# Performance work log

Hardware: AMD Instinct MI355X
Metric: run time of the kernel (lower is better)

The kernel has to match this reference:

```python
import jax, jax.numpy as jnp
import numpy as np

TAU = 0.1
MASK_VAL = 1e9


def setup_inputs() -> dict:
    key = jax.random.key(0)
    ka, kb = jax.random.split(key)
    B, D = 4096, 512
    return {
        "view_a": jax.random.normal(ka, (B, D), dtype=jnp.float32),
        "view_b": jax.random.normal(kb, (B, D), dtype=jnp.float32),
    }


def _l2norm(x):
    return x / jnp.maximum(jnp.linalg.norm(x, axis=-1, keepdims=True), 1e-12)


def reference(view_a, view_b):
    a = _l2norm(view_a)
    b = _l2norm(view_b)
    B = a.shape[0]
    labels = jnp.arange(B)  # start_i = 0 (single device)
    mask = jnp.eye(B, dtype=a.dtype) * MASK_VAL

    logits_aa = a @ a.T / TAU - mask
    logits_bb = b @ b.T / TAU - mask
    logits_ab = a @ b.T / TAU
    logits_ba = b @ a.T / TAU

    full_a = jnp.concatenate([logits_ab, logits_aa], axis=1)  # [B, 2B]
    full_b = jnp.concatenate([logits_ba, logits_bb], axis=1)

    def ce(logits):
        logp = jax.nn.log_softmax(logits, axis=-1)
        return -jnp.mean(jnp.take_along_axis(logp, labels[:, None], axis=-1))

    loss = (ce(full_a) + ce(full_b)) / 2

    pred = jnp.argmax(full_a, axis=-1)
    acc = 100.0 * jnp.sum(pred == labels) / B
    return loss, acc
```

## Files before the change

kernel.cpp:

```cpp
#include <hip/hip_runtime.h>
#include <stdint.h>


#define BN 4096
#define DK 512
#define NEG_BIG -1e30f
#define SCL 0.15625f
#define SCL2 0.225396744f
#define C2 14.4269504f
#define TILE_BYTES (64 * DK)
#define NCHUNK 32

typedef __attribute__((ext_vector_type(16))) float floatx16;
typedef __attribute__((ext_vector_type(8))) int intx8;

__global__ void __launch_bounds__(256) prep_kernel(
    const float* __restrict__ A, const float* __restrict__ Bv,
    unsigned char* __restrict__ Gn, float* __restrict__ diag,
    float* __restrict__ out, float* __restrict__ zbase,
    float* __restrict__ mbase) {
  const int gtid = blockIdx.x * 256 + threadIdx.x;
  if (gtid < 2) out[gtid] = 0.0f;
  for (int idx = gtid; idx < (NCHUNK + 64) * 8192; idx += 1024 * 256)
    zbase[idx] = 0.0f;
  for (int idx = gtid; idx < (NCHUNK + 32) * 4096; idx += 1024 * 256)
    mbase[idx] = NEG_BIG;

  const int w = threadIdx.x >> 6, lane = threadIdx.x & 63;
  const int row = blockIdx.x * 4 + w;
  const float4* pa4 = (const float4*)(A + (size_t)row * DK);
  const float4* pb4 = (const float4*)(Bv + (size_t)row * DK);
  float4 a0 = pa4[lane * 2], a1 = pa4[lane * 2 + 1];
  float4 b0 = pb4[lane * 2], b1 = pb4[lane * 2 + 1];
  float ssa = a0.x * a0.x + a0.y * a0.y + a0.z * a0.z + a0.w * a0.w +
              a1.x * a1.x + a1.y * a1.y + a1.z * a1.z + a1.w * a1.w;
  float ssb = b0.x * b0.x + b0.y * b0.y + b0.z * b0.z + b0.w * b0.w +
              b1.x * b1.x + b1.y * b1.y + b1.z * b1.z + b1.w * b1.w;
  float sab = a0.x * b0.x + a0.y * b0.y + a0.z * b0.z + a0.w * b0.w +
              a1.x * b1.x + a1.y * b1.y + a1.z * b1.z + a1.w * b1.w;
#pragma unroll
  for (int off = 32; off > 0; off >>= 1) {
    ssa += __shfl_xor(ssa, off);
    ssb += __shfl_xor(ssb, off);
    sab += __shfl_xor(sab, off);
  }
  float na = fmaxf(sqrtf(ssa), 1e-12f);
  float nb = fmaxf(sqrtf(ssb), 1e-12f);
  const float s = 8.0f;
  float sa = s / na, sb = s / nb;
  const int doff = (lane >> 2) * 32 + (lane & 1) * 16 + ((lane >> 1) & 1) * 8;
  {
    int v0 = __builtin_amdgcn_cvt_pk_fp8_f32(a0.x * sa, a0.y * sa, 0, false);
    v0 = __builtin_amdgcn_cvt_pk_fp8_f32(a0.z * sa, a0.w * sa, v0, true);
    int v1 = __builtin_amdgcn_cvt_pk_fp8_f32(a1.x * sa, a1.y * sa, 0, false);
    v1 = __builtin_amdgcn_cvt_pk_fp8_f32(a1.z * sa, a1.w * sa, v1, true);
    int2 pv; pv.x = v0; pv.y = v1;
    *(int2*)(Gn + (size_t)row * DK + doff) = pv;
  }
  {
    int v0 = __builtin_amdgcn_cvt_pk_fp8_f32(b0.x * sb, b0.y * sb, 0, false);
    v0 = __builtin_amdgcn_cvt_pk_fp8_f32(b0.z * sb, b0.w * sb, v0, true);
    int v1 = __builtin_amdgcn_cvt_pk_fp8_f32(b1.x * sb, b1.y * sb, 0, false);
    v1 = __builtin_amdgcn_cvt_pk_fp8_f32(b1.z * sb, b1.w * sb, v1, true);
    int2 pv; pv.x = v0; pv.y = v1;
    *(int2*)(Gn + (size_t)(BN + row) * DK + doff) = pv;
  }
  if (lane == 0) diag[row] = (sab / (na * nb)) * 10.0f;
}

__global__ void __launch_bounds__(256, 2) tiles_kernel(
    const unsigned char* __restrict__ Gn,
    float* __restrict__ pRS, float* __restrict__ pCS,
    float* __restrict__ pRM, float* __restrict__ pCM) {
  __shared__ __align__(16) unsigned char smem[TILE_BYTES + 4096];

  int bid = blockIdx.x, I = 0;
  for (;;) {
    const int nc = (131 - 2 * I) >> 2;
    if (bid < nc) break;
    bid -= nc; ++I;
  }
  const int chunk = bid;
  const int j0 = 2 * I + chunk * 4;
  const int ntiles = min(4, 128 - 2 * I - chunk * 4);

  const int tid = threadIdx.x;
  const int lane = tid & 63, w = tid >> 6;
  const int n5 = lane & 31, h = lane >> 5;
  const int rbase = I * 128 + w * 32;

  intx8 aw[8];
  {
    const unsigned char* p = Gn + (size_t)(rbase + n5) * DK + h * 16;
#pragma unroll
    for (int i = 0; i < 8; ++i) {
      int4 c0 = *(const int4*)(p + i * 64);
      int4 c1 = *(const int4*)(p + i * 64 + 32);
      intx8 v = {c0.x, c0.y, c0.z, c0.w, c1.x, c1.y, c1.z, c1.w};
      aw[i] = v;
    }
  }

  auto stage = [&](int j) {
    const int cb = j * 64;
#pragma unroll
    for (int ii = 0; ii < 8; ++ii) {
      const int cp = w * 8 + ii;
      const int cl = cp * 2 + h;
      const unsigned char* src =
          Gn + (size_t)(cb + cl) * DK + ((n5 ^ (cl & 31)) * 16);
      __builtin_amdgcn_global_load_lds(
          (const __attribute__((address_space(1))) void*)src,
          (__attribute__((address_space(3))) void*)(smem + cp * 1024),
          16, 0, 0);
    }
  };

  float l[16], mxr[16];
#pragma unroll
  for (int r = 0; r < 16; ++r) { l[r] = 0.f; mxr[r] = NEG_BIG; }

  float* T = (float*)(smem + TILE_BYTES);

#pragma unroll 1
  for (int t = 0; t < ntiles; ++t) {
    const int j = j0 + t;
    stage(j);
    __syncthreads();

    floatx16 acc[2];
#pragma unroll
    for (int cs = 0; cs < 2; ++cs)
#pragma unroll
      for (int r = 0; r < 16; ++r) acc[cs][r] = 0.f;

    const unsigned char* bbase = smem + (size_t)n5 * DK;
#pragma unroll
    for (int i = 0; i < 8; ++i) {
      const int p1 = ((4 * i + h) ^ n5) * 16;
      const int p2 = ((4 * i + 2 + h) ^ n5) * 16;
#pragma unroll
      for (int cs = 0; cs < 2; ++cs) {
        int4 b0 = *(const int4*)(bbase + cs * 32 * DK + p1);
        int4 b1 = *(const int4*)(bbase + cs * 32 * DK + p2);
        intx8 bw = {b0.x, b0.y, b0.z, b0.w, b1.x, b1.y, b1.z, b1.w};
        acc[cs] = __builtin_amdgcn_mfma_scale_f32_32x32x64_f8f6f4(
            aw[i], bw, acc[cs], 0, 0, 0, 0x7F7F7F7F, 0, 0x7F7F7F7F);
      }
    }

    const int cbase = j * 64;
    const bool diagp = ((j >> 1) == I);
    const bool lblp = (I < 32) && (j >= 64);
    const int colg0 = cbase + n5, colg1 = cbase + 32 + n5;
    float csum0 = 0.f, csum1 = 0.f, cmax0 = NEG_BIG, cmax1 = NEG_BIG;

#define EPI_BODY(EXCL0_EXPR, EXCL1_EXPR)                                    \
  _Pragma("unroll")                                                         \
  for (int r = 0; r < 16; ++r) {                                            \
    const int rowg = rbase + (r & 3) + 8 * (r >> 2) + 4 * h;                \
    (void)rowg;                                                             \
    {                                                                       \
      const float v = acc[0][r];                                            \
      const bool excl = (EXCL0_EXPR);                                       \
      const float e = excl ? 0.f : exp2f(fmaf(v, SCL2, -C2));               \
      const float vm = excl ? NEG_BIG : v;                                  \
      l[r] += e; mxr[r] = fmaxf(mxr[r], vm);                                \
      csum0 += e; cmax0 = fmaxf(cmax0, vm);                                 \
    }                                                                       \
    {                                                                       \
      const float v = acc[1][r];                                            \
      const bool excl = (EXCL1_EXPR);                                       \
      const float e = excl ? 0.f : exp2f(fmaf(v, SCL2, -C2));               \
      const float vm = excl ? NEG_BIG : v;                                  \
      l[r] += e; mxr[r] = fmaxf(mxr[r], vm);                                \
      csum1 += e; cmax1 = fmaxf(cmax1, vm);                                 \
    }                                                                       \
  }

    if (diagp) {
      EPI_BODY(colg0 <= rowg, colg1 <= rowg)
    } else if (lblp) {
      EPI_BODY(colg0 == rowg + BN, colg1 == rowg + BN)
    } else {
      EPI_BODY(false, false)
    }
#undef EPI_BODY

    csum0 += __shfl_xor(csum0, 32);
    csum1 += __shfl_xor(csum1, 32);
    cmax0 = fmaxf(cmax0, __shfl_xor(cmax0, 32));
    cmax1 = fmaxf(cmax1, __shfl_xor(cmax1, 32));
    float* cps = T;
    float* cpm = T + 256;
    if (h == 0) {
      cps[w * 64 + n5] = csum0; cps[w * 64 + 32 + n5] = csum1;
      cpm[w * 64 + n5] = cmax0; cpm[w * 64 + 32 + n5] = cmax1;
    }
    __syncthreads();
    if (tid < 64) {
      const float s =
          cps[tid] + cps[64 + tid] + cps[128 + tid] + cps[192 + tid];
      pCS[(size_t)I * 8192 + cbase + tid] = s;
      if (j < 64) {
        const float m = fmaxf(fmaxf(cpm[tid], cpm[64 + tid]),
                              fmaxf(cpm[128 + tid], cpm[192 + tid]));
        pCM[(size_t)I * 4096 + cbase + tid] = m;
      }
    }
  }

#pragma unroll
  for (int off = 1; off < 32; off <<= 1)
#pragma unroll
    for (int r = 0; r < 16; ++r) l[r] += __shfl_xor(l[r], off);
  if (I < 32) {
#pragma unroll
    for (int off = 1; off < 32; off <<= 1)
#pragma unroll
      for (int r = 0; r < 16; ++r)
        mxr[r] = fmaxf(mxr[r], __shfl_xor(mxr[r], off));
  }
  if (n5 == 0) {
#pragma unroll
    for (int r = 0; r < 16; ++r) {
      const int rowg = rbase + (r & 3) + 8 * (r >> 2) + 4 * h;
      pRS[(size_t)chunk * 8192 + rowg] = l[r];
      if (I < 32) pRM[(size_t)chunk * 4096 + rowg] = mxr[r];
    }
  }
}

__global__ void __launch_bounds__(256) finalize_kernel(
    const float* __restrict__ pRS, const float* __restrict__ pCS,
    const float* __restrict__ pRM, const float* __restrict__ pCM,
    const float* __restrict__ diag, float* __restrict__ out) {
  const int i = blockIdx.x * 256 + threadIdx.x;
  float SA = 0.f, SB = 0.f, MA = NEG_BIG;
  for (int s = 0; s < NCHUNK; ++s) {
    SA += pRS[(size_t)s * 8192 + i];
    SB += pRS[(size_t)s * 8192 + BN + i];
  }
  for (int s = 0; s < 64; ++s) {
    SA += pCS[(size_t)s * 8192 + i];
    SB += pCS[(size_t)s * 8192 + BN + i];
  }
  for (int s = 0; s < NCHUNK; ++s) MA = fmaxf(MA, pRM[(size_t)s * 4096 + i]);
  for (int s = 0; s < 32; ++s)     MA = fmaxf(MA, pCM[(size_t)s * 4096 + i]);
  MA *= SCL;

  const float d = diag[i];
  const float eL = exp2f(fmaf(d, 1.44269504f, -C2));
  float lseA = 10.0f + logf(SA + eL);
  float lseB = 10.0f + logf(SB + eL);
  float lossi = (lseA - d) + (lseB - d);
  float corr = (d >= MA) ? 1.f : 0.f;
#pragma unroll
  for (int off = 32; off > 0; off >>= 1) {
    lossi += __shfl_xor(lossi, off);
    corr += __shfl_xor(corr, off);
  }
  __shared__ float sred[2][4];
  if ((threadIdx.x & 63) == 0) {
    int w = threadIdx.x >> 6;
    sred[0][w] = lossi; sred[1][w] = corr;
  }
  __syncthreads();
  if (threadIdx.x == 0) {
    float ls = sred[0][0] + sred[0][1] + sred[0][2] + sred[0][3];
    float cs = sred[1][0] + sred[1][1] + sred[1][2] + sred[1][3];
    atomicAdd(&out[0], ls * (1.0f / 8192.0f));
    atomicAdd(&out[1], cs * (100.0f / 4096.0f));
  }
}

extern "C" void kernel_launch(void* const* d_in, const int* in_sizes, int n_in,
                              void* d_out, int out_size, void* d_ws, size_t ws_size,
                              hipStream_t stream) {
  const float* A = (const float*)d_in[0];
  const float* Bv = (const float*)d_in[1];
  unsigned char* Gn = (unsigned char*)d_ws;
  float* diag = (float*)(Gn + (size_t)8192 * DK);
  float* pRS = diag + BN;
  float* pCS = pRS + NCHUNK * 8192;
  float* pRM = pCS + 64 * 8192;
  float* pCM = pRM + NCHUNK * 4096;
  float* out = (float*)d_out;

  prep_kernel<<<BN / 4, 256, 0, stream>>>(A, Bv, Gn, diag, out, pRS, pRM);
  tiles_kernel<<<1056, 256, 0, stream>>>(Gn, pRS, pCS, pRM, pCM);
  finalize_kernel<<<BN / 256, 256, 0, stream>>>(pRS, pCS, pRM, pCM, diag, out);
}
```

Baseline: 118.4 us.

## Replace per-chunk partial buffers with global atomic row sums and maxima

The partial row/column sum and max buffers are replaced by single global arrays updated with atomicAdd and an order-preserving encoded atomicMax. This removes the large zero/fill initialisation in prep and the multi-pass reduction in finalize. Work per block drops from four tiles to two, which roughly doubles the grid to 2080 blocks for better load balance. In exchange it adds atomic contention and a nondeterministic summation order.

```diff
diff --git a/kernel.cpp b/kernel.cpp
--- a/kernel.cpp
+++ b/kernel.cpp
@@ -9,22 +9,29 @@
 #define SCL2 0.225396744f
 #define C2 14.4269504f
 #define TILE_BYTES (64 * DK)
-#define NCHUNK 32
+#define NBLK2 2080
 
 typedef __attribute__((ext_vector_type(16))) float floatx16;
 typedef __attribute__((ext_vector_type(8))) int intx8;
+
+__device__ __forceinline__ unsigned encf(float f) {
+  unsigned u = __float_as_uint(f);
+  return ((int)u < 0) ? ~u : (u | 0x80000000u);
+}
+__device__ __forceinline__ float decf(unsigned u) {
+  return (u & 0x80000000u) ? __uint_as_float(u & 0x7FFFFFFFu)
+                           : __uint_as_float(~u);
+}
 
 __global__ void __launch_bounds__(256) prep_kernel(
     const float* __restrict__ A, const float* __restrict__ Bv,
     unsigned char* __restrict__ Gn, float* __restrict__ diag,
-    float* __restrict__ out, float* __restrict__ zbase,
-    float* __restrict__ mbase) {
+    float* __restrict__ out, float* __restrict__ SAB,
+    unsigned* __restrict__ MaxEnc) {
   const int gtid = blockIdx.x * 256 + threadIdx.x;
   if (gtid < 2) out[gtid] = 0.0f;
-  for (int idx = gtid; idx < (NCHUNK + 64) * 8192; idx += 1024 * 256)
-    zbase[idx] = 0.0f;
-  for (int idx = gtid; idx < (NCHUNK + 32) * 4096; idx += 1024 * 256)
-    mbase[idx] = NEG_BIG;
+  if (gtid < 2 * BN) SAB[gtid] = 0.0f;
+  if (gtid < BN) MaxEnc[gtid] = encf(NEG_BIG);
 
   const int w = threadIdx.x >> 6, lane = threadIdx.x & 63;
   const int row = blockIdx.x * 4 + w;
@@ -70,19 +77,17 @@
 
 __global__ void __launch_bounds__(256, 2) tiles_kernel(
     const unsigned char* __restrict__ Gn,
-    float* __restrict__ pRS, float* __restrict__ pCS,
-    float* __restrict__ pRM, float* __restrict__ pCM) {
-  __shared__ __align__(16) unsigned char smem[TILE_BYTES + 4096];
+    float* __restrict__ SAB, unsigned* __restrict__ MaxEnc) {
+  __shared__ __align__(16) unsigned char smem[TILE_BYTES + 2048];
 
   int bid = blockIdx.x, I = 0;
   for (;;) {
-    const int nc = (131 - 2 * I) >> 2;
+    const int nc = 64 - I;
     if (bid < nc) break;
     bid -= nc; ++I;
   }
   const int chunk = bid;
-  const int j0 = 2 * I + chunk * 4;
-  const int ntiles = min(4, 128 - 2 * I - chunk * 4);
+  const int j0 = 2 * I + chunk * 2;
 
   const int tid = threadIdx.x;
   const int lane = tid & 63, w = tid >> 6;
@@ -123,7 +128,7 @@
   float* T = (float*)(smem + TILE_BYTES);
 
 #pragma unroll 1
-  for (int t = 0; t < ntiles; ++t) {
+  for (int t = 0; t < 2; ++t) {
     const int j = j0 + t;
     stage(j);
     __syncthreads();
@@ -201,11 +206,11 @@
     if (tid < 64) {
       const float s =
           cps[tid] + cps[64 + tid] + cps[128 + tid] + cps[192 + tid];
-      pCS[(size_t)I * 8192 + cbase + tid] = s;
+      atomicAdd(&SAB[cbase + tid], s);
       if (j < 64) {
         const float m = fmaxf(fmaxf(cpm[tid], cpm[64 + tid]),
                               fmaxf(cpm[128 + tid], cpm[192 + tid]));
-        pCM[(size_t)I * 4096 + cbase + tid] = m;
+        atomicMax(&MaxEnc[cbase + tid], encf(m));
       }
     }
   }
@@ -225,29 +230,19 @@
 #pragma unroll
     for (int r = 0; r < 16; ++r) {
       const int rowg = rbase + (r & 3) + 8 * (r >> 2) + 4 * h;
-      pRS[(size_t)chunk * 8192 + rowg] = l[r];
-      if (I < 32) pRM[(size_t)chunk * 4096 + rowg] = mxr[r];
+      atomicAdd(&SAB[rowg], l[r]);
+      if (I < 32) atomicMax(&MaxEnc[rowg], encf(mxr[r]));
     }
   }
 }
 
 __global__ void __launch_bounds__(256) finalize_kernel(
-    const float* __restrict__ pRS, const float* __restrict__ pCS,
-    const float* __restrict__ pRM, const float* __restrict__ pCM,
+    const float* __restrict__ SAB, const unsigned* __restrict__ MaxEnc,
     const float* __restrict__ diag, float* __restrict__ out) {
   const int i = blockIdx.x * 256 + threadIdx.x;
-  float SA = 0.f, SB = 0.f, MA = NEG_BIG;
-  for (int s = 0; s < NCHUNK; ++s) {
-    SA += pRS[(size_t)s * 8192 + i];
-    SB += pRS[(size_t)s * 8192 + BN + i];
-  }
-  for (int s = 0; s < 64; ++s) {
-    SA += pCS[(size_t)s * 8192 + i];
-    SB += pCS[(size_t)s * 8192 + BN + i];
-  }
-  for (int s = 0; s < NCHUNK; ++s) MA = fmaxf(MA, pRM[(size_t)s * 4096 + i]);
-  for (int s = 0; s < 32; ++s)     MA = fmaxf(MA, pCM[(size_t)s * 4096 + i]);
-  MA *= SCL;
+  const float SA = SAB[i];
+  const float SB = SAB[BN + i];
+  const float MA = decf(MaxEnc[i]) * SCL;
 
   const float d = diag[i];
   const float eL = exp2f(fmaf(d, 1.44269504f, -C2));
@@ -281,13 +276,11 @@
   const float* Bv = (const float*)d_in[1];
   unsigned char* Gn = (unsigned char*)d_ws;
   float* diag = (float*)(Gn + (size_t)8192 * DK);
-  float* pRS = diag + BN;
-  float* pCS = pRS + NCHUNK * 8192;
-  float* pRM = pCS + 64 * 8192;
-  float* pCM = pRM + NCHUNK * 4096;
+  float* SAB = diag + BN;
+  unsigned* MaxEnc = (unsigned*)(SAB + 2 * BN);
   float* out = (float*)d_out;
 
-  prep_kernel<<<BN / 4, 256, 0, stream>>>(A, Bv, Gn, diag, out, pRS, pRM);
-  tiles_kernel<<<1056, 256, 0, stream>>>(Gn, pRS, pCS, pRM, pCM);
-  finalize_kernel<<<BN / 256, 256, 0, stream>>>(pRS, pCS, pRM, pCM, diag, out);
-}
+  prep_kernel<<<BN / 4, 256, 0, stream>>>(A, Bv, Gn, diag, out, SAB, MaxEnc);
+  tiles_kernel<<<NBLK2, 256, 0, stream>>>(Gn, SAB, MaxEnc);
+  finalize_kernel<<<BN / 256, 256, 0, stream>>>(SAB, MaxEnc, diag, out);
+}
```

After: 152.5 us. 28.8% more time.

## Widen tile chunks to eight per block and parallelize finalize reduction

Applied to the files above, without the earlier changes.

Each tiles block now processes up to eight column tiles instead of four, halving the block count and the number of row partial-sum slices. The row-stat smem scratch shrinks accordingly. The finalize kernel splits each row's partial reduction across eight lanes with shuffle combining and launches more blocks, so the serial per-thread loop over partial slices is shorter. Fewer, longer tile blocks may reduce load balance across CUs and lengthen the tail.

```diff
diff --git a/kernel.cpp b/kernel.cpp
--- a/kernel.cpp
+++ b/kernel.cpp
@@ -9,7 +9,8 @@
 #define SCL2 0.225396744f
 #define C2 14.4269504f
 #define TILE_BYTES (64 * DK)
-#define NCHUNK 32
+#define NRS 16
+#define NBLK 544
 
 typedef __attribute__((ext_vector_type(16))) float floatx16;
 typedef __attribute__((ext_vector_type(8))) int intx8;
@@ -21,9 +22,9 @@
     float* __restrict__ mbase) {
   const int gtid = blockIdx.x * 256 + threadIdx.x;
   if (gtid < 2) out[gtid] = 0.0f;
-  for (int idx = gtid; idx < (NCHUNK + 64) * 8192; idx += 1024 * 256)
+  for (int idx = gtid; idx < (NRS + 64) * 8192; idx += 1024 * 256)
     zbase[idx] = 0.0f;
-  for (int idx = gtid; idx < (NCHUNK + 32) * 4096; idx += 1024 * 256)
+  for (int idx = gtid; idx < (NRS + 32) * 4096; idx += 1024 * 256)
     mbase[idx] = NEG_BIG;
 
   const int w = threadIdx.x >> 6, lane = threadIdx.x & 63;
@@ -72,17 +73,17 @@
     const unsigned char* __restrict__ Gn,
     float* __restrict__ pRS, float* __restrict__ pCS,
     float* __restrict__ pRM, float* __restrict__ pCM) {
-  __shared__ __align__(16) unsigned char smem[TILE_BYTES + 4096];
+  __shared__ __align__(16) unsigned char smem[TILE_BYTES + 2048];
 
   int bid = blockIdx.x, I = 0;
   for (;;) {
-    const int nc = (131 - 2 * I) >> 2;
+    const int nc = (135 - 2 * I) >> 3;
     if (bid < nc) break;
     bid -= nc; ++I;
   }
   const int chunk = bid;
-  const int j0 = 2 * I + chunk * 4;
-  const int ntiles = min(4, 128 - 2 * I - chunk * 4);
+  const int j0 = 2 * I + chunk * 8;
+  const int ntiles = min(8, 128 - 2 * I - chunk * 8);
 
   const int tid = threadIdx.x;
   const int lane = tid & 63, w = tid >> 6;
@@ -235,26 +236,43 @@
     const float* __restrict__ pRS, const float* __restrict__ pCS,
     const float* __restrict__ pRM, const float* __restrict__ pCM,
     const float* __restrict__ diag, float* __restrict__ out) {
-  const int i = blockIdx.x * 256 + threadIdx.x;
+  const int k = threadIdx.x & 7;
+  const int r = threadIdx.x >> 3;
+  const int i = blockIdx.x * 32 + r;
+
   float SA = 0.f, SB = 0.f, MA = NEG_BIG;
-  for (int s = 0; s < NCHUNK; ++s) {
+#pragma unroll
+  for (int q = 0; q < 2; ++q) {
+    const int s = k * 2 + q;
     SA += pRS[(size_t)s * 8192 + i];
     SB += pRS[(size_t)s * 8192 + BN + i];
-  }
-  for (int s = 0; s < 64; ++s) {
+    MA = fmaxf(MA, pRM[(size_t)s * 4096 + i]);
+  }
+#pragma unroll
+  for (int q = 0; q < 8; ++q) {
+    const int s = k * 8 + q;
     SA += pCS[(size_t)s * 8192 + i];
     SB += pCS[(size_t)s * 8192 + BN + i];
   }
-  for (int s = 0; s < NCHUNK; ++s) MA = fmaxf(MA, pRM[(size_t)s * 4096 + i]);
-  for (int s = 0; s < 32; ++s)     MA = fmaxf(MA, pCM[(size_t)s * 4096 + i]);
-  MA *= SCL;
-
-  const float d = diag[i];
-  const float eL = exp2f(fmaf(d, 1.44269504f, -C2));
-  float lseA = 10.0f + logf(SA + eL);
-  float lseB = 10.0f + logf(SB + eL);
-  float lossi = (lseA - d) + (lseB - d);
-  float corr = (d >= MA) ? 1.f : 0.f;
+#pragma unroll
+  for (int q = 0; q < 4; ++q) {
+    const int s = k * 4 + q;
+    MA = fmaxf(MA, pCM[(size_t)s * 4096 + i]);
+  }
+#pragma unroll
+  for (int off = 1; off < 8; off <<= 1) {
+    SA += __shfl_xor(SA, off);
+    SB += __shfl_xor(SB, off);
+    MA = fmaxf(MA, __shfl_xor(MA, off));
+  }
+
+  float lossi = 0.f, corr = 0.f;
+  if (k == 0) {
+    const float d = diag[i];
+    const float eL = exp2f(fmaf(d, 1.44269504f, -C2));
+    lossi = (10.0f + logf(SA + eL) - d) + (10.0f + logf(SB + eL) - d);
+    corr = (d >= MA * SCL) ? 1.f : 0.f;
+  }
 #pragma unroll
   for (int off = 32; off > 0; off >>= 1) {
     lossi += __shfl_xor(lossi, off);
@@ -282,12 +300,12 @@
   unsigned char* Gn = (unsigned char*)d_ws;
   float* diag = (float*)(Gn + (size_t)8192 * DK);
   float* pRS = diag + BN;
-  float* pCS = pRS + NCHUNK * 8192;
+  float* pCS = pRS + NRS * 8192;
   float* pRM = pCS + 64 * 8192;
-  float* pCM = pRM + NCHUNK * 4096;
+  float* pCM = pRM + NRS * 4096;
   float* out = (float*)d_out;
 
   prep_kernel<<<BN / 4, 256, 0, stream>>>(A, Bv, Gn, diag, out, pRS, pRM);
-  tiles_kernel<<<1056, 256, 0, stream>>>(Gn, pRS, pCS, pRM, pCM);
-  finalize_kernel<<<BN / 256, 256, 0, stream>>>(pRS, pCS, pRM, pCM, diag, out);
+  tiles_kernel<<<NBLK, 256, 0, stream>>>(Gn, pRS, pCS, pRM, pCM);
+  finalize_kernel<<<BN / 32, 256, 0, stream>>>(pRS, pCS, pRM, pCM, diag, out);
 }
```

After: 116.5 us. About the same (-1.6%).
